# Optimization experiments

Hardware: AMD Instinct MI355X
Metric: run time of the kernel (lower is better)

The kernel has to match this reference:

```python
import jax, jax.numpy as jnp
import numpy as np

N_NODES = 20000
N_EDGES = 200000
N_GRAPHS = 128
IN_DIM = 16
EDGE_DIM = 8
HID = 64
OUT_DIM = 10


def setup_inputs() -> dict:
    key = jax.random.key(0)
    ks = jax.random.split(key, 16)
    s = lambda k, *shape: jax.random.normal(k, shape, dtype=jnp.float32) * 0.05
    edge_attr = jax.random.normal(ks[0], (N_EDGES, EDGE_DIM), dtype=jnp.float32)
    edge_index = jax.random.randint(ks[1], (2, N_EDGES), 0, N_NODES, dtype=jnp.int32)
    batch = jnp.sort(jax.random.randint(ks[2], (N_NODES,), 0, N_GRAPHS, dtype=jnp.int32))
    return {
        "edge_attr": edge_attr,
        "edge_index": edge_index,
        "batch": batch,
        # node embedding (single row, repeated since data.x is None)
        "node_emb": s(ks[3], 1, IN_DIM),
        # edge MLP: edge_dim -> hid -> hid -> in*hid
        "w1": s(ks[4], EDGE_DIM, HID), "b1": jnp.zeros((HID,), jnp.float32),
        "w2": s(ks[5], HID, HID), "b2": jnp.zeros((HID,), jnp.float32),
        "w3": s(ks[6], HID, IN_DIM * HID), "b3": jnp.zeros((IN_DIM * HID,), jnp.float32),
        # NNConv root weight (Linear, bias=False) and conv bias
        "root_w": s(ks[7], IN_DIM, HID),
        "conv_b": jnp.zeros((HID,), jnp.float32),
        # classifier head: hid -> 2*hid -> out
        "l1_w": s(ks[8], HID, 2 * HID), "l1_b": jnp.zeros((2 * HID,), jnp.float32),
        "l2_w": s(ks[9], 2 * HID, OUT_DIM), "l2_b": jnp.zeros((OUT_DIM,), jnp.float32),
    }


def reference(edge_attr, edge_index, batch, node_emb, w1, b1, w2, b2, w3, b3,
              root_w, conv_b, l1_w, l1_b, l2_w, l2_b):
    # node features: single embedding row repeated for every node
    x = jnp.broadcast_to(node_emb, (N_NODES, IN_DIM))  # [N, in]

    # edge MLP -> dynamic per-edge weight matrices [E, in, hid]
    h = jax.nn.relu(edge_attr @ w1 + b1)
    h = jax.nn.relu(h @ w2 + b2)
    theta = (h @ w3 + b3).reshape(N_EDGES, IN_DIM, HID)

    src, dst = edge_index[0], edge_index[1]
    # per-edge matmul: gather source features, apply edge weight
    msg = jnp.einsum('ei,eih->eh', x[src], theta)  # [E, hid]
    # scatter-add aggregate at destination nodes
    agg = jax.ops.segment_sum(msg, dst, num_segments=N_NODES)  # [N, hid]

    # NNConv root transform + bias, then relu
    out = jax.nn.relu(agg + x @ root_w + conv_b)  # [N, hid]

    # global mean pool per graph
    sums = jax.ops.segment_sum(out, batch, num_segments=N_GRAPHS)  # [G, hid]
    counts = jax.ops.segment_sum(jnp.ones((N_NODES,), out.dtype), batch,
                                 num_segments=N_GRAPHS)
    pooled = sums / jnp.maximum(counts, 1.0)[:, None]

    # classifier head
    logits = jax.nn.relu(pooled @ l1_w + l1_b) @ l2_w + l2_b  # [G, out]
    return logits
```

## Files before the change

### kernel.cpp

```cpp
#include <hip/hip_runtime.h>
#include <hip/hip_bf16.h>
#include <hip/amd_detail/amd_hip_unsafe_atomics.h>

#define N_EDGES 200000
#define N_NODES 20000
#define N_GRAPHS 128
#define IN_DIM 16
#define EDGE_DIM 8
#define HID 64
#define OUT_DIM 10
#define SCAN_NBLK ((N_NODES + 1023) / 1024)
#define N_TILES (N_EDGES / 16)
#define TPW 2
#define N_EWAVES (N_TILES / TPW)

typedef __attribute__((ext_vector_type(8))) short bf16x8;
typedef __attribute__((ext_vector_type(4))) float f32x4;

__device__ __forceinline__ ushort f2bf(float x) {
    unsigned b = __float_as_uint(x);
    return (ushort)((b + 0x7FFFu + ((b >> 16) & 1u)) >> 16);
}
__device__ __forceinline__ float bf2f(ushort u) {
    return __uint_as_float(((unsigned)u) << 16);
}

__global__ __launch_bounds__(256) void combo_kernel(
    const float* __restrict__ emb, const float* __restrict__ w3,
    const float* __restrict__ b3, const float* __restrict__ root_w,
    const float* __restrict__ conv_b, const int* __restrict__ dst_idx,
    const float* __restrict__ w1, const float* __restrict__ w2,
    float* __restrict__ W3p, float* __restrict__ b3p, float* __restrict__ r,
    ushort* __restrict__ fw1, ushort* __restrict__ fw2,
    int* __restrict__ counts)
{
    if (blockIdx.x < 16) {
        int t = blockIdx.x * 256 + threadIdx.x;
        int k = t >> 6;
        int h = t & 63;
        float acc = 0.f;
#pragma unroll
        for (int i = 0; i < IN_DIM; ++i)
            acc = fmaf(emb[i], w3[k * (IN_DIM * HID) + i * HID + h], acc);
        W3p[t] = acc;
        if (t < HID) {
            float a = 0.f, rr = 0.f;
#pragma unroll
            for (int i = 0; i < IN_DIM; ++i) {
                a  = fmaf(emb[i], b3[i * HID + t], a);
                rr = fmaf(emb[i], root_w[i * HID + t], rr);
            }
            b3p[t] = a;
            r[t]   = rr + conv_b[t];
        }
    } else if (blockIdx.x < 64) {
        int idx  = (blockIdx.x - 16) * 256 + threadIdx.x;
        int frag = idx >> 9;
        int rem  = idx & 511;
        int lane = rem >> 3, i = rem & 7;
        int q = lane >> 4, n16 = lane & 15;
        if (frag < 8) {
            int t = frag >> 1, h = frag & 1;
            int k = 8 * q + i, n = t * 16 + n16;
            float v = (k < EDGE_DIM) ? w1[k * HID + n] : 0.f;
            ushort hi = f2bf(v);
            fw1[((t * 2 + h) * 64 + lane) * 8 + i] =
                (h == 0) ? hi : f2bf(v - bf2f(hi));
        } else {
            int u = frag - 8;
            int t = u >> 2, f = (u >> 1) & 1, h = u & 1;
            int k = f * 32 + 8 * q + i, n = t * 16 + n16;
            float v = w2[k * HID + n];
            ushort hi = f2bf(v);
            fw2[(((t * 2 + f) * 2 + h) * 64 + lane) * 8 + i] =
                (h == 0) ? hi : f2bf(v - bf2f(hi));
        }
    } else {
        int e = (blockIdx.x - 64) * 256 + threadIdx.x;
        if (e < N_EDGES) atomicAdd(&counts[dst_idx[e]], 1);
    }
}

__global__ __launch_bounds__(1024) void scanA_kernel(
    const int* __restrict__ counts, int* __restrict__ start, int* __restrict__ tot,
    const float* __restrict__ W3p, ushort* __restrict__ fw3)
{
    const int b = blockIdx.x, t = threadIdx.x;
    if (b >= SCAN_NBLK) {
        int idx  = (b - SCAN_NBLK) * 1024 + t;
        int u    = idx >> 9;
        int rem  = idx & 511;
        int lane = rem >> 3, i = rem & 7;
        int tt = u >> 2, f = (u >> 1) & 1, h = u & 1;
        int k = f * 32 + 8 * (lane >> 4) + i, n = tt * 16 + (lane & 15);
        float v = W3p[k * HID + n];
        ushort hi = f2bf(v);
        fw3[(((tt * 2 + f) * 2 + h) * 64 + lane) * 8 + i] =
            (h == 0) ? hi : f2bf(v - bf2f(hi));
        return;
    }
    const int i = b * 1024 + t;
    const int v = (i < N_NODES) ? counts[i] : 0;
    const int lane = t & 63, wid = t >> 6;
    __shared__ int wsum[16];
    int incl = v;
#pragma unroll
    for (int off = 1; off < 64; off <<= 1) {
        int u = __shfl_up(incl, off, 64);
        if (lane >= off) incl += u;
    }
    if (lane == 63) wsum[wid] = incl;
    __syncthreads();
    if (wid == 0) {
        int wv = (lane < 16) ? wsum[lane] : 0;
        int wi = wv;
#pragma unroll
        for (int off = 1; off < 16; off <<= 1) {
            int u = __shfl_up(wi, off, 64);
            if (lane >= off) wi += u;
        }
        if (lane < 16) wsum[lane] = wi - wv;
    }
    __syncthreads();
    const int excl = wsum[wid] + incl - v;
    if (i < N_NODES) start[i] = excl;
    if (t == 1023) tot[b] = excl + v;
}

__global__ __launch_bounds__(1024) void scanC_kernel(
    int* __restrict__ start, int* __restrict__ cursor, const int* __restrict__ tot)
{
    __shared__ int s_off;
    const int b = blockIdx.x, t = threadIdx.x;
    if (t < 64) {
        int v = (t < b && t < SCAN_NBLK) ? tot[t] : 0;
#pragma unroll
        for (int o = 32; o >= 1; o >>= 1) v += __shfl_xor(v, o, 64);
        if (t == 0) s_off = v;
    }
    __syncthreads();
    const int i = b * 1024 + t;
    if (i < N_NODES) {
        const int s = start[i] + s_off;
        start[i]  = s;
        cursor[i] = s;
    }
    if (b == 0 && t == 0) start[N_NODES] = N_EDGES;
}

__global__ __launch_bounds__(256) void edge_mfma_kernel(
    const float* __restrict__ edge_attr, const int* __restrict__ dst_idx,
    const ushort* __restrict__ fw1, const ushort* __restrict__ fw2,
    const ushort* __restrict__ fw3,
    const float* __restrict__ b1, const float* __restrict__ b2,
    const float* __restrict__ b3p,
    int* __restrict__ cursor, ushort* __restrict__ msg16)
{
    const int lane = threadIdx.x & 63;
    const int wv   = threadIdx.x >> 6;
    const int gw   = blockIdx.x * 4 + wv;
    const int tile0 = gw * TPW;
    if (tile0 >= N_TILES) return;
    const int q = lane >> 4, l16 = lane & 15;

    __shared__ ushort s_hi[4][TPW][16][72];
    __shared__ ushort s_lo[4][TPW][16][72];

    float bb1[4], bb2[4], bb3[4];
#pragma unroll
    for (int t = 0; t < 4; ++t) {
        bb1[t] = b1[t * 16 + l16];
        bb2[t] = b2[t * 16 + l16];
        bb3[t] = b3p[t * 16 + l16];
    }

    float e8[TPW][8];
    int   p_mine[TPW];
#pragma unroll
    for (int tt = 0; tt < TPW; ++tt) {
        p_mine[tt] = 0;
#pragma unroll
        for (int i = 0; i < 8; ++i) e8[tt][i] = 0.f;
        if (lane < 16) {
            const long em = (long)(tile0 + tt) * 16 + lane;
            const float4 A = *(const float4*)&edge_attr[em * EDGE_DIM + 0];
            const float4 B = *(const float4*)&edge_attr[em * EDGE_DIM + 4];
            e8[tt][0] = A.x; e8[tt][1] = A.y; e8[tt][2] = A.z; e8[tt][3] = A.w;
            e8[tt][4] = B.x; e8[tt][5] = B.y; e8[tt][6] = B.z; e8[tt][7] = B.w;
            p_mine[tt] = atomicAdd(&cursor[dst_idx[em]], 1);
        }
    }

    {
        bf16x8 w1h[4], w1l[4];
#pragma unroll
        for (int t = 0; t < 4; ++t) {
            w1h[t] = ((const bf16x8*)fw1)[(t * 2 + 0) * 64 + lane];
            w1l[t] = ((const bf16x8*)fw1)[(t * 2 + 1) * 64 + lane];
        }
#pragma unroll
        for (int tt = 0; tt < TPW; ++tt) {
            bf16x8 a1h, a1l;
#pragma unroll
            for (int i = 0; i < 8; ++i) {
                const ushort hi = f2bf(e8[tt][i]);
                a1h[i] = (short)hi;
                a1l[i] = (short)f2bf(e8[tt][i] - bf2f(hi));
            }
#pragma unroll
            for (int t = 0; t < 4; ++t) {
                f32x4 c = {0.f, 0.f, 0.f, 0.f};
                c = __builtin_amdgcn_mfma_f32_16x16x32_bf16(a1l, w1h[t], c, 0, 0, 0);
                c = __builtin_amdgcn_mfma_f32_16x16x32_bf16(a1h, w1l[t], c, 0, 0, 0);
                c = __builtin_amdgcn_mfma_f32_16x16x32_bf16(a1h, w1h[t], c, 0, 0, 0);
#pragma unroll
                for (int rr = 0; rr < 4; ++rr) {
                    float x = fmaxf(c[rr] + bb1[t], 0.f);
                    const ushort hi = f2bf(x);
                    s_hi[wv][tt][q * 4 + rr][t * 16 + l16] = hi;
                    s_lo[wv][tt][q * 4 + rr][t * 16 + l16] = f2bf(x - bf2f(hi));
                }
            }
        }
    }

    {
        bf16x8 w2h[4][2], w2l[4][2];
#pragma unroll
        for (int t = 0; t < 4; ++t)
#pragma unroll
            for (int f = 0; f < 2; ++f) {
                w2h[t][f] = ((const bf16x8*)fw2)[((t * 2 + f) * 2 + 0) * 64 + lane];
                w2l[t][f] = ((const bf16x8*)fw2)[((t * 2 + f) * 2 + 1) * 64 + lane];
            }
#pragma unroll
        for (int tt = 0; tt < TPW; ++tt) {
            bf16x8 a2h[2], a2l[2];
#pragma unroll
            for (int f = 0; f < 2; ++f) {
                a2h[f] = *(const bf16x8*)&s_hi[wv][tt][l16][f * 32 + 8 * q];
                a2l[f] = *(const bf16x8*)&s_lo[wv][tt][l16][f * 32 + 8 * q];
            }
            f32x4 cc[4];
#pragma unroll
            for (int t = 0; t < 4; ++t) {
                f32x4 c = {0.f, 0.f, 0.f, 0.f};
#pragma unroll
                for (int f = 0; f < 2; ++f) {
                    c = __builtin_amdgcn_mfma_f32_16x16x32_bf16(a2l[f], w2h[t][f], c, 0, 0, 0);
                    c = __builtin_amdgcn_mfma_f32_16x16x32_bf16(a2h[f], w2l[t][f], c, 0, 0, 0);
                    c = __builtin_amdgcn_mfma_f32_16x16x32_bf16(a2h[f], w2h[t][f], c, 0, 0, 0);
                }
                cc[t] = c;
            }
#pragma unroll
            for (int t = 0; t < 4; ++t)
#pragma unroll
                for (int rr = 0; rr < 4; ++rr) {
                    float x = fmaxf(cc[t][rr] + bb2[t], 0.f);
                    const ushort hi = f2bf(x);
                    s_hi[wv][tt][q * 4 + rr][t * 16 + l16] = hi;
                    s_lo[wv][tt][q * 4 + rr][t * 16 + l16] = f2bf(x - bf2f(hi));
                }
        }
    }

    {
        bf16x8 w3h[4][2], w3l[4][2];
#pragma unroll
        for (int t = 0; t < 4; ++t)
#pragma unroll
            for (int f = 0; f < 2; ++f) {
                w3h[t][f] = ((const bf16x8*)fw3)[((t * 2 + f) * 2 + 0) * 64 + lane];
                w3l[t][f] = ((const bf16x8*)fw3)[((t * 2 + f) * 2 + 1) * 64 + lane];
            }
#pragma unroll
        for (int tt = 0; tt < TPW; ++tt) {
            bf16x8 a3h[2], a3l[2];
#pragma unroll
            for (int f = 0; f < 2; ++f) {
                a3h[f] = *(const bf16x8*)&s_hi[wv][tt][l16][f * 32 + 8 * q];
                a3l[f] = *(const bf16x8*)&s_lo[wv][tt][l16][f * 32 + 8 * q];
            }
            f32x4 cc[4];
#pragma unroll
            for (int t = 0; t < 4; ++t) {
                f32x4 c = {0.f, 0.f, 0.f, 0.f};
#pragma unroll
                for (int f = 0; f < 2; ++f) {
                    c = __builtin_amdgcn_mfma_f32_16x16x32_bf16(a3l[f], w3h[t][f], c, 0, 0, 0);
                    c = __builtin_amdgcn_mfma_f32_16x16x32_bf16(a3h[f], w3l[t][f], c, 0, 0, 0);
                    c = __builtin_amdgcn_mfma_f32_16x16x32_bf16(a3h[f], w3h[t][f], c, 0, 0, 0);
                }
                cc[t] = c;
            }
            int p_r[4];
#pragma unroll
            for (int rr = 0; rr < 4; ++rr)
                p_r[rr] = __shfl(p_mine[tt], q * 4 + rr);
#pragma unroll
            for (int t = 0; t < 4; ++t)
#pragma unroll
                for (int rr = 0; rr < 4; ++rr)
                    msg16[(long)p_r[rr] * HID + t * 16 + l16] =
                        f2bf(cc[t][rr] + bb3[t]);
        }
    }
}

#define GN_PER_WAVE 8
__global__ __launch_bounds__(256) void gather_kernel(
    const ushort* __restrict__ msg16, const int* __restrict__ start,
    const float* __restrict__ r, const int* __restrict__ batch,
    float* __restrict__ sums, float* __restrict__ counts_f)
{
    const int wave = threadIdx.x >> 6;
    const int j    = threadIdx.x & 63;
    const int n0   = blockIdx.x * (4 * GN_PER_WAVE) + wave * GN_PER_WAVE;
    if (n0 >= N_NODES) return;
    const int n1 = min(n0 + GN_PER_WAVE, N_NODES);
    const float rj = r[j];

    int   g    = batch[n0];
    float pacc = 0.f, cnt = 0.f;
    for (int n = n0; n < n1; ++n) {
        const int gn = batch[n];
        if (gn != g) {
            unsafeAtomicAdd(&sums[g * HID + j], pacc);
            if (j == 0) unsafeAtomicAdd(&counts_f[g], cnt);
            g = gn; pacc = 0.f; cnt = 0.f;
        }
        float acc = 0.f;
        const int p0 = start[n], p1 = start[n + 1];
        for (int p = p0; p < p1; ++p)
            acc += bf2f(msg16[(long)p * HID + j]);
        pacc += fmaxf(acc + rj, 0.f);
        cnt  += 1.f;
    }
    unsafeAtomicAdd(&sums[g * HID + j], pacc);
    if (j == 0) unsafeAtomicAdd(&counts_f[g], cnt);
}

__global__ __launch_bounds__(128) void head_kernel(
    const float* __restrict__ sums, const float* __restrict__ counts,
    const float* __restrict__ l1_w, const float* __restrict__ l1_b,
    const float* __restrict__ l2_w, const float* __restrict__ l2_b,
    float* __restrict__ out)
{
    const int g = blockIdx.x;
    const int t = threadIdx.x;
    __shared__ float pooled[HID];
    __shared__ float hid[2 * HID];

    const float cnt = fmaxf(counts[g], 1.0f);
    if (t < HID) pooled[t] = sums[g * HID + t] / cnt;
    __syncthreads();

    float a = l1_b[t];
#pragma unroll
    for (int k = 0; k < HID; ++k)
        a = fmaf(pooled[k], l1_w[k * (2 * HID) + t], a);
    hid[t] = fmaxf(a, 0.f);
    __syncthreads();

    if (t < OUT_DIM) {
        float o = l2_b[t];
#pragma unroll
        for (int k = 0; k < 2 * HID; ++k)
            o = fmaf(hid[k], l2_w[k * OUT_DIM + t], o);
        out[g * OUT_DIM + t] = o;
    }
}

extern "C" void kernel_launch(void* const* d_in, const int* in_sizes, int n_in,
                              void* d_out, int out_size, void* d_ws, size_t ws_size,
                              hipStream_t stream) {
    const float* edge_attr = (const float*)d_in[0];
    const int*   edge_idx  = (const int*)d_in[1];
    const int*   batch     = (const int*)d_in[2];
    const float* node_emb  = (const float*)d_in[3];
    const float* w1        = (const float*)d_in[4];
    const float* b1        = (const float*)d_in[5];
    const float* w2        = (const float*)d_in[6];
    const float* b2        = (const float*)d_in[7];
    const float* w3        = (const float*)d_in[8];
    const float* b3        = (const float*)d_in[9];
    const float* root_w    = (const float*)d_in[10];
    const float* conv_b    = (const float*)d_in[11];
    const float* l1_w      = (const float*)d_in[12];
    const float* l1_b      = (const float*)d_in[13];
    const float* l2_w      = (const float*)d_in[14];
    const float* l2_b      = (const float*)d_in[15];
    float* out = (float*)d_out;

    float* ws     = (float*)d_ws;
    float* W3p    = ws;
    float* b3p    = W3p + HID * HID;
    float* r      = b3p + HID;
    float* sums   = r + HID;
    float* cts    = sums + N_GRAPHS * HID;
    int*   counts = (int*)(cts + N_GRAPHS);
    int*   startp = counts + N_NODES;
    int*   cursor = startp + (N_NODES + 1);
    int*   tot    = cursor + N_NODES;
    ushort* fw1 = (ushort*)(((uintptr_t)(tot + SCAN_NBLK) + 15) & ~(uintptr_t)15);
    ushort* fw2 = fw1 + 4096;
    ushort* fw3 = fw2 + 8192;
    ushort* msg16 = fw3 + 8192;

    hipMemsetAsync(sums, 0,
                   (size_t)(N_GRAPHS * HID + N_GRAPHS + N_NODES) * 4, stream);

    const int* dst_idx = edge_idx + N_EDGES;

    combo_kernel<<<64 + (N_EDGES + 255) / 256, 256, 0, stream>>>(
        node_emb, w3, b3, root_w, conv_b, dst_idx, w1, w2,
        W3p, b3p, r, fw1, fw2, counts);

    scanA_kernel<<<SCAN_NBLK + 8, 1024, 0, stream>>>(counts, startp, tot, W3p, fw3);
    scanC_kernel<<<SCAN_NBLK, 1024, 0, stream>>>(startp, cursor, tot);

    edge_mfma_kernel<<<(N_EWAVES + 3) / 4, 256, 0, stream>>>(
        edge_attr, dst_idx, fw1, fw2, fw3, b1, b2, b3p, cursor, msg16);

    gather_kernel<<<(N_NODES + 4 * GN_PER_WAVE - 1) / (4 * GN_PER_WAVE), 256, 0, stream>>>(
        msg16, startp, r, batch, sums, cts);

    head_kernel<<<N_GRAPHS, 128, 0, stream>>>(
        sums, cts, l1_w, l1_b, l2_w, l2_b, out);
}
```

Before: 94.42 us.

## Fuse two-pass scan into single kernel with decoupled chained block offsets

Merges the two scan kernels into one by passing running block totals through a global turn counter and accumulator, so blocks serialize only on a single thread. The zeroing of pooled sums moves into an extra block of that kernel, which shrinks the memset. Gather nodes per wave drop from 8 to 2 for more parallelism. This saves one kernel launch and one global pass over start, but it depends on earlier blocks being scheduled before later ones spin-wait, which holds here because only 20 blocks are launched.

```diff
diff --git a/kernel.cpp b/kernel.cpp
--- a/kernel.cpp
+++ b/kernel.cpp
@@ -81,28 +81,38 @@
     }
 }
 
-__global__ __launch_bounds__(1024) void scanA_kernel(
-    const int* __restrict__ counts, int* __restrict__ start, int* __restrict__ tot,
-    const float* __restrict__ W3p, ushort* __restrict__ fw3)
+__global__ __launch_bounds__(1024) void scan_kernel(
+    const int* __restrict__ counts, int* __restrict__ start,
+    int* __restrict__ cursor,
+    const float* __restrict__ W3p, ushort* __restrict__ fw3,
+    float* __restrict__ sums_zero, int* __restrict__ turn,
+    int* __restrict__ run)
 {
     const int b = blockIdx.x, t = threadIdx.x;
     if (b >= SCAN_NBLK) {
-        int idx  = (b - SCAN_NBLK) * 1024 + t;
-        int u    = idx >> 9;
-        int rem  = idx & 511;
-        int lane = rem >> 3, i = rem & 7;
-        int tt = u >> 2, f = (u >> 1) & 1, h = u & 1;
-        int k = f * 32 + 8 * (lane >> 4) + i, n = tt * 16 + (lane & 15);
-        float v = W3p[k * HID + n];
-        ushort hi = f2bf(v);
-        fw3[(((tt * 2 + f) * 2 + h) * 64 + lane) * 8 + i] =
-            (h == 0) ? hi : f2bf(v - bf2f(hi));
+        int ab = b - SCAN_NBLK;
+        if (ab < 8) {
+            int idx  = ab * 1024 + t;
+            int u    = idx >> 9;
+            int rem  = idx & 511;
+            int lane = rem >> 3, i = rem & 7;
+            int tt = u >> 2, f = (u >> 1) & 1, h = u & 1;
+            int k = f * 32 + 8 * (lane >> 4) + i, n = tt * 16 + (lane & 15);
+            float v = W3p[k * HID + n];
+            ushort hi = f2bf(v);
+            fw3[(((tt * 2 + f) * 2 + h) * 64 + lane) * 8 + i] =
+                (h == 0) ? hi : f2bf(v - bf2f(hi));
+        } else {
+            for (int i = t; i < N_GRAPHS * HID + N_GRAPHS; i += 1024)
+                sums_zero[i] = 0.f;
+        }
         return;
     }
     const int i = b * 1024 + t;
     const int v = (i < N_NODES) ? counts[i] : 0;
     const int lane = t & 63, wid = t >> 6;
     __shared__ int wsum[16];
+    __shared__ int s_base;
     int incl = v;
 #pragma unroll
     for (int off = 1; off < 64; off <<= 1) {
@@ -123,28 +133,18 @@
     }
     __syncthreads();
     const int excl = wsum[wid] + incl - v;
-    if (i < N_NODES) start[i] = excl;
-    if (t == 1023) tot[b] = excl + v;
-}
-
-__global__ __launch_bounds__(1024) void scanC_kernel(
-    int* __restrict__ start, int* __restrict__ cursor, const int* __restrict__ tot)
-{
-    __shared__ int s_off;
-    const int b = blockIdx.x, t = threadIdx.x;
-    if (t < 64) {
-        int v = (t < b && t < SCAN_NBLK) ? tot[t] : 0;
-#pragma unroll
-        for (int o = 32; o >= 1; o >>= 1) v += __shfl_xor(v, o, 64);
-        if (t == 0) s_off = v;
+    if (t == 1023) {
+        while (__hip_atomic_load(turn, __ATOMIC_ACQUIRE,
+                                 __HIP_MEMORY_SCOPE_AGENT) != b) {}
+        const int base = *run;
+        *run = base + excl + v;
+        __hip_atomic_store(turn, b + 1, __ATOMIC_RELEASE,
+                           __HIP_MEMORY_SCOPE_AGENT);
+        s_base = base;
     }
     __syncthreads();
-    const int i = b * 1024 + t;
-    if (i < N_NODES) {
-        const int s = start[i] + s_off;
-        start[i]  = s;
-        cursor[i] = s;
-    }
+    const int s = s_base + excl;
+    if (i < N_NODES) { start[i] = s; cursor[i] = s; }
     if (b == 0 && t == 0) start[N_NODES] = N_EDGES;
 }
 
@@ -308,7 +308,7 @@
     }
 }
 
-#define GN_PER_WAVE 8
+#define GN_PER_WAVE 2
 __global__ __launch_bounds__(256) void gather_kernel(
     const ushort* __restrict__ msg16, const int* __restrict__ start,
     const float* __restrict__ r, const int* __restrict__ batch,
@@ -400,16 +400,16 @@
     float* sums   = r + HID;
     float* cts    = sums + N_GRAPHS * HID;
     int*   counts = (int*)(cts + N_GRAPHS);
-    int*   startp = counts + N_NODES;
+    int*   turn   = counts + N_NODES;
+    int*   run    = turn + 1;
+    int*   startp = run + 1;
     int*   cursor = startp + (N_NODES + 1);
-    int*   tot    = cursor + N_NODES;
-    ushort* fw1 = (ushort*)(((uintptr_t)(tot + SCAN_NBLK) + 15) & ~(uintptr_t)15);
+    ushort* fw1 = (ushort*)(((uintptr_t)(cursor + N_NODES) + 15) & ~(uintptr_t)15);
     ushort* fw2 = fw1 + 4096;
     ushort* fw3 = fw2 + 8192;
     ushort* msg16 = fw3 + 8192;
 
-    hipMemsetAsync(sums, 0,
-                   (size_t)(N_GRAPHS * HID + N_GRAPHS + N_NODES) * 4, stream);
+    hipMemsetAsync(counts, 0, (size_t)(N_NODES + 2) * 4, stream);
 
     const int* dst_idx = edge_idx + N_EDGES;
 
@@ -417,8 +417,8 @@
         node_emb, w3, b3, root_w, conv_b, dst_idx, w1, w2,
         W3p, b3p, r, fw1, fw2, counts);
 
-    scanA_kernel<<<SCAN_NBLK + 8, 1024, 0, stream>>>(counts, startp, tot, W3p, fw3);
-    scanC_kernel<<<SCAN_NBLK, 1024, 0, stream>>>(startp, cursor, tot);
+    scan_kernel<<<SCAN_NBLK + 9, 1024, 0, stream>>>(
+        counts, startp, cursor, W3p, fw3, sums, turn, run);
 
     edge_mfma_kernel<<<(N_EWAVES + 3) / 4, 256, 0, stream>>>(
         edge_attr, dst_idx, fw1, fw2, fw3, b1, b2, b3p, cursor, msg16);
```

New measurement: 127.9 us. 35.5% more time.
